# Kernel optimization log

Measured on AMD Instinct MI355X. Metric: run time of the kernel, lower is better.

Reference implementation:

```python
import jax, jax.numpy as jnp
import numpy as np
import math

FEATURE_DIMS = 6
D_HIDDEN = 32
N_TOKENS = 2097152
NUM_SEGMENTS = 8192
SCALE = 400.0 / math.log(10.0)


def setup_inputs() -> dict:
    key = jax.random.key(0)
    ks = jax.random.split(key, 8)
    x = jax.random.normal(ks[0], (N_TOKENS, FEATURE_DIMS), dtype=jnp.float32)
    segment_ids = jnp.sort(jax.random.randint(ks[1], (N_TOKENS,), 0, NUM_SEGMENTS)).astype(jnp.int32)
    # params (kaiming-ish init, same layout as nn.Linear: y = x @ W.T + b -> stored pre-transposed)
    W1 = jax.random.normal(ks[2], (FEATURE_DIMS, D_HIDDEN), dtype=jnp.float32) / np.sqrt(FEATURE_DIMS)
    b1 = jax.random.normal(ks[3], (D_HIDDEN,), dtype=jnp.float32) * 0.01
    wr = jax.random.normal(ks[4], (D_HIDDEN,), dtype=jnp.float32) / np.sqrt(D_HIDDEN)
    br = jax.random.normal(ks[5], (), dtype=jnp.float32) * 0.01
    wz = jax.random.normal(ks[6], (D_HIDDEN,), dtype=jnp.float32) / np.sqrt(D_HIDDEN)
    bz = jax.random.normal(ks[7], (), dtype=jnp.float32) * 0.01
    return {"x": x, "W1": W1, "b1": b1, "wr": wr, "br": br, "wz": wz, "bz": bz,
            "segment_ids": segment_ids, "num_segments": NUM_SEGMENTS}


def reference(x, W1, b1, wr, br, wz, bz, segment_ids, num_segments):
    # layer1: Linear + ReLU  -> h [N, d_hidden]
    h = jax.nn.relu(x @ W1 + b1)
    # rating / weight heads, squeezed to [N]
    r = h @ wr + br
    z = h @ wz + bz
    # per-segment (per-game) softmax over z, weighted sum of r -- single pass, no Python loop
    zmax = jax.ops.segment_max(z, segment_ids, num_segments=num_segments)  # [G], -inf for empty
    e = jnp.exp(z - zmax[segment_ids])                                      # [N]
    num = jax.ops.segment_sum(e * r, segment_ids, num_segments=num_segments)  # [G]
    den = jax.ops.segment_sum(e, segment_ids, num_segments=num_segments)      # [G]
    den_safe = jnp.where(den > 0, den, 1.0)
    preds = jnp.where(den > 0, num / den_safe, 0.0)  # empty segment -> 0, as in the torch code
    return SCALE * preds
```

## Files before the change

kernel.cpp:

```cpp
#include <hip/hip_runtime.h>

#define SCALE_F 173.71779276130078f
#define BLOCK 256
#define TPT 4

typedef float v2f __attribute__((ext_vector_type(2)));

__global__ void zero_ws_kernel(float* __restrict__ ws, int n) {
    int i = blockIdx.x * 256 + threadIdx.x;
    if (i < n) ws[i] = 0.0f;
}

__global__ __launch_bounds__(BLOCK, 8) void strength_main_kernel(
    const float* __restrict__ x,
    const float* __restrict__ W1,
    const float* __restrict__ b1,
    const float* __restrict__ wr,
    const float* __restrict__ brp,
    const float* __restrict__ wz,
    const float* __restrict__ bzp,
    const int*   __restrict__ seg,
    int N,
    float* __restrict__ num,
    float* __restrict__ den)
{
    const int tid  = threadIdx.x;
    const int lane = tid & 63;

    const int t0   = blockIdx.x * (BLOCK * TPT) + tid * TPT;
    const int kmax = (t0 >= N) ? 0 : ((N - t0 < TPT) ? (N - t0) : TPT);

    float a[TPT * 6];
    int   sg[TPT];
    if (kmax == TPT) {
        const float4* xp = (const float4*)(x + (size_t)t0 * 6);
        #pragma unroll
        for (int i = 0; i < 6; ++i) {
            float4 v = xp[i];
            a[4 * i + 0] = v.x; a[4 * i + 1] = v.y;
            a[4 * i + 2] = v.z; a[4 * i + 3] = v.w;
        }
        int4 s0v = *(const int4*)(seg + t0);
        sg[0] = s0v.x; sg[1] = s0v.y; sg[2] = s0v.z; sg[3] = s0v.w;
    } else {
        #pragma unroll
        for (int k = 0; k < TPT; ++k) {
            if (k < kmax) {
                const float* xp = x + (size_t)(t0 + k) * 6;
                #pragma unroll
                for (int i = 0; i < 6; ++i) a[k * 6 + i] = xp[i];
                sg[k] = seg[t0 + k];
            } else {
                #pragma unroll
                for (int i = 0; i < 6; ++i) a[k * 6 + i] = 0.0f;
                sg[k] = -1;
            }
        }
    }

    v2f X[2][6];
    #pragma unroll
    for (int p = 0; p < 2; ++p)
        #pragma unroll
        for (int f = 0; f < 6; ++f)
            X[p][f] = (v2f){ a[(2*p)*6 + f], a[(2*p+1)*6 + f] };

    const float brv = *brp;
    const float bzv = *bzp;

    v2f R[2], Z[2];
    R[0] = (v2f){brv, brv}; R[1] = (v2f){brv, brv};
    Z[0] = (v2f){bzv, bzv}; Z[1] = (v2f){bzv, bzv};

    #pragma unroll 2
    for (int c = 0; c < 16; ++c) {
        const float2 w0 = *(const float2*)&W1[0 * 32 + 2 * c];
        const float2 w1 = *(const float2*)&W1[1 * 32 + 2 * c];
        const float2 w2 = *(const float2*)&W1[2 * 32 + 2 * c];
        const float2 w3 = *(const float2*)&W1[3 * 32 + 2 * c];
        const float2 w4 = *(const float2*)&W1[4 * 32 + 2 * c];
        const float2 w5 = *(const float2*)&W1[5 * 32 + 2 * c];
        const float2 bb = *(const float2*)&b1[2 * c];
        const float2 rr = *(const float2*)&wr[2 * c];
        const float2 zz = *(const float2*)&wz[2 * c];

        #pragma unroll
        for (int j = 0; j < 2; ++j) {
            const float wj0 = j ? w0.y : w0.x;
            const float wj1 = j ? w1.y : w1.x;
            const float wj2 = j ? w2.y : w2.x;
            const float wj3 = j ? w3.y : w3.x;
            const float wj4 = j ? w4.y : w4.x;
            const float wj5 = j ? w5.y : w5.x;
            const float bbj = j ? bb.y : bb.x;
            const float rrj = j ? rr.y : rr.x;
            const float zzj = j ? zz.y : zz.x;
            const v2f vw0 = (v2f){wj0, wj0}, vw1 = (v2f){wj1, wj1};
            const v2f vw2 = (v2f){wj2, wj2}, vw3 = (v2f){wj3, wj3};
            const v2f vw4 = (v2f){wj4, wj4}, vw5 = (v2f){wj5, wj5};
            const v2f vbb = (v2f){bbj, bbj};
            const v2f vrr = (v2f){rrj, rrj}, vzz = (v2f){zzj, zzj};
            #pragma unroll
            for (int p = 0; p < 2; ++p) {
                v2f h = X[p][0]*vw0 + (X[p][1]*vw1 + (X[p][2]*vw2 +
                        (X[p][3]*vw3 + (X[p][4]*vw4 + (X[p][5]*vw5 + vbb)))));
                h = __builtin_elementwise_max(h, (v2f){0.f, 0.f});
                R[p] = h * vrr + R[p];
                Z[p] = h * vzz + Z[p];
            }
        }
    }

    float rv[TPT] = { R[0].x, R[0].y, R[1].x, R[1].y };
    float zv[TPT] = { Z[0].x, Z[0].y, Z[1].x, Z[1].y };

    int   key = (kmax > 0) ? sg[0] : -1;
    float E = 0.0f, ER = 0.0f;
    #pragma unroll
    for (int k = 0; k < TPT; ++k) {
        if (k < kmax) {
            float e = __expf(zv[k]);
            if (sg[k] != key) {
                atomicAdd(&den[key], E);
                atomicAdd(&num[key], ER);
                key = sg[k]; E = 0.0f; ER = 0.0f;
            }
            E += e; ER = fmaf(e, rv[k], ER);
        }
    }

    #pragma unroll
    for (int d = 1; d < 64; d <<= 1) {
        int   k2 = __shfl_up(key, d);
        float E2 = __shfl_up(E,   d);
        float R2 = __shfl_up(ER,  d);
        if (lane >= d && k2 == key) { E += E2; ER += R2; }
    }
    int knext = __shfl_down(key, 1);
    bool last = (lane == 63) || (knext != key);
    if (last && key >= 0) {
        atomicAdd(&den[key], E);
        atomicAdd(&num[key], ER);
    }
}

__global__ void finalize_kernel(const float* __restrict__ num,
                                const float* __restrict__ den,
                                float* __restrict__ out, int G) {
    int g = blockIdx.x * 256 + threadIdx.x;
    if (g < G) {
        float d = den[g];
        out[g] = (d > 0.0f) ? (SCALE_F * num[g] / d) : 0.0f;
    }
}

extern "C" void kernel_launch(void* const* d_in, const int* in_sizes, int n_in,
                              void* d_out, int out_size, void* d_ws, size_t ws_size,
                              hipStream_t stream) {
    const float* x   = (const float*)d_in[0];
    const float* W1  = (const float*)d_in[1];
    const float* b1  = (const float*)d_in[2];
    const float* wr  = (const float*)d_in[3];
    const float* br  = (const float*)d_in[4];
    const float* wz  = (const float*)d_in[5];
    const float* bz  = (const float*)d_in[6];
    const int*   seg = (const int*)d_in[7];

    int N = in_sizes[7];
    int G = out_size;

    float* num = (float*)d_ws;
    float* den = num + G;
    float* out = (float*)d_out;

    int zn = 2 * G;
    zero_ws_kernel<<<(zn + 255) / 256, 256, 0, stream>>>(num, zn);

    long tokens_per_block = (long)BLOCK * TPT;
    int  nblocks = (int)(((long)N + tokens_per_block - 1) / tokens_per_block);
    strength_main_kernel<<<nblocks, BLOCK, 0, stream>>>(
        x, W1, b1, wr, br, wz, bz, seg, N, num, den);

    finalize_kernel<<<(G + 255) / 256, 256, 0, stream>>>(num, den, out, G);
}
```

Before: 28.88 us.

## Stage x through swizzled LDS with coalesced loads and halve tokens per thread

Cuts tokens per thread from four to two, which doubles the number of blocks. Each block now loads its slice of x with fully coalesced float4 reads into XOR-swizzled shared memory, and each thread then reads its own 24-byte rows back from LDS. Before, every thread read its six float4s directly, so accesses across the wavefront were strided. The cost is an added barrier, LDS traffic, and twice as many blocks and segment atomics.

```diff
diff --git a/kernel.cpp b/kernel.cpp
--- a/kernel.cpp
+++ b/kernel.cpp
@@ -2,7 +2,8 @@
 
 #define SCALE_F 173.71779276130078f
 #define BLOCK 256
-#define TPT 4
+#define TPT 2
+#define TOK_PER_BLOCK (BLOCK * TPT)
 
 typedef float v2f __attribute__((ext_vector_type(2)));
 
@@ -10,6 +11,8 @@
     int i = blockIdx.x * 256 + threadIdx.x;
     if (i < n) ws[i] = 0.0f;
 }
+
+__device__ __forceinline__ int swz(int q) { return q ^ ((q >> 3) & 7); }
 
 __global__ __launch_bounds__(BLOCK, 8) void strength_main_kernel(
     const float* __restrict__ x,
@@ -24,25 +27,36 @@
     float* __restrict__ num,
     float* __restrict__ den)
 {
-    const int tid  = threadIdx.x;
-    const int lane = tid & 63;
+    __shared__ float4 xs[TOK_PER_BLOCK * 6 / 4];
 
-    const int t0   = blockIdx.x * (BLOCK * TPT) + tid * TPT;
-    const int kmax = (t0 >= N) ? 0 : ((N - t0 < TPT) ? (N - t0) : TPT);
+    const int tid    = threadIdx.x;
+    const int lane   = tid & 63;
+    const int bstart = blockIdx.x * TOK_PER_BLOCK;
+    const int t0     = bstart + tid * TPT;
 
     float a[TPT * 6];
     int   sg[TPT];
-    if (kmax == TPT) {
-        const float4* xp = (const float4*)(x + (size_t)t0 * 6);
+    int   kmax;
+
+    if (bstart + TOK_PER_BLOCK <= N) {
+        kmax = TPT;
+        const float4* xg = (const float4*)(x + (size_t)bstart * 6);
         #pragma unroll
-        for (int i = 0; i < 6; ++i) {
-            float4 v = xp[i];
-            a[4 * i + 0] = v.x; a[4 * i + 1] = v.y;
-            a[4 * i + 2] = v.z; a[4 * i + 3] = v.w;
+        for (int i = 0; i < 3; ++i) {
+            int q = tid + BLOCK * i;
+            xs[swz(q)] = xg[q];
         }
-        int4 s0v = *(const int4*)(seg + t0);
-        sg[0] = s0v.x; sg[1] = s0v.y; sg[2] = s0v.z; sg[3] = s0v.w;
+        __syncthreads();
+        float4 v0 = xs[swz(3 * tid + 0)];
+        float4 v1 = xs[swz(3 * tid + 1)];
+        float4 v2 = xs[swz(3 * tid + 2)];
+        a[0] = v0.x; a[1]  = v0.y; a[2]  = v0.z; a[3]  = v0.w;
+        a[4] = v1.x; a[5]  = v1.y; a[6]  = v1.z; a[7]  = v1.w;
+        a[8] = v2.x; a[9]  = v2.y; a[10] = v2.z; a[11] = v2.w;
+        int2 s2 = *(const int2*)(seg + t0);
+        sg[0] = s2.x; sg[1] = s2.y;
     } else {
+        kmax = (t0 >= N) ? 0 : ((N - t0 < TPT) ? (N - t0) : TPT);
         #pragma unroll
         for (int k = 0; k < TPT; ++k) {
             if (k < kmax) {
@@ -58,19 +72,15 @@
         }
     }
 
-    v2f X[2][6];
+    v2f X[6];
     #pragma unroll
-    for (int p = 0; p < 2; ++p)
-        #pragma unroll
-        for (int f = 0; f < 6; ++f)
-            X[p][f] = (v2f){ a[(2*p)*6 + f], a[(2*p+1)*6 + f] };
+    for (int f = 0; f < 6; ++f) X[f] = (v2f){ a[f], a[6 + f] };
 
     const float brv = *brp;
     const float bzv = *bzp;
 
-    v2f R[2], Z[2];
-    R[0] = (v2f){brv, brv}; R[1] = (v2f){brv, brv};
-    Z[0] = (v2f){bzv, bzv}; Z[1] = (v2f){bzv, bzv};
+    v2f R = (v2f){brv, brv};
+    v2f Z = (v2f){bzv, bzv};
 
     #pragma unroll 2
     for (int c = 0; c < 16; ++c) {
@@ -100,19 +110,16 @@
             const v2f vw4 = (v2f){wj4, wj4}, vw5 = (v2f){wj5, wj5};
             const v2f vbb = (v2f){bbj, bbj};
             const v2f vrr = (v2f){rrj, rrj}, vzz = (v2f){zzj, zzj};
-            #pragma unroll
-            for (int p = 0; p < 2; ++p) {
-                v2f h = X[p][0]*vw0 + (X[p][1]*vw1 + (X[p][2]*vw2 +
-                        (X[p][3]*vw3 + (X[p][4]*vw4 + (X[p][5]*vw5 + vbb)))));
-                h = __builtin_elementwise_max(h, (v2f){0.f, 0.f});
-                R[p] = h * vrr + R[p];
-                Z[p] = h * vzz + Z[p];
-            }
+            v2f h = X[0]*vw0 + (X[1]*vw1 + (X[2]*vw2 +
+                    (X[3]*vw3 + (X[4]*vw4 + (X[5]*vw5 + vbb)))));
+            h = __builtin_elementwise_max(h, (v2f){0.f, 0.f});
+            R = h * vrr + R;
+            Z = h * vzz + Z;
         }
     }
 
-    float rv[TPT] = { R[0].x, R[0].y, R[1].x, R[1].y };
-    float zv[TPT] = { Z[0].x, Z[0].y, Z[1].x, Z[1].y };
+    float rv[TPT] = { R.x, R.y };
+    float zv[TPT] = { Z.x, Z.y };
 
     int   key = (kmax > 0) ? sg[0] : -1;
     float E = 0.0f, ER = 0.0f;
@@ -176,8 +183,7 @@
     int zn = 2 * G;
     zero_ws_kernel<<<(zn + 255) / 256, 256, 0, stream>>>(num, zn);
 
-    long tokens_per_block = (long)BLOCK * TPT;
-    int  nblocks = (int)(((long)N + tokens_per_block - 1) / tokens_per_block);
+    int nblocks = (int)(((long)N + TOK_PER_BLOCK - 1) / TOK_PER_BLOCK);
     strength_main_kernel<<<nblocks, BLOCK, 0, stream>>>(
         x, W1, b1, wr, br, wz, bz, seg, N, num, den);
 
```

New measurement: 30.89 us. 7.0% more time.

## Fuse finalize into main kernel via last-block ticket and use memset

Applied to the files above, without the earlier changes.

Removes the separate finalize kernel: each block bumps a global ticket counter after its atomics drain, and the last block to finish computes num/den for all segments. The zeroing kernel is replaced by hipMemsetAsync covering the accumulators and the ticket. This saves kernel launches and inter-kernel gaps, but the whole finalize (8192 segments) now runs serially on one block at the tail.

```diff
diff --git a/kernel.cpp b/kernel.cpp
--- a/kernel.cpp
+++ b/kernel.cpp
@@ -5,11 +5,6 @@
 #define TPT 4
 
 typedef float v2f __attribute__((ext_vector_type(2)));
-
-__global__ void zero_ws_kernel(float* __restrict__ ws, int n) {
-    int i = blockIdx.x * 256 + threadIdx.x;
-    if (i < n) ws[i] = 0.0f;
-}
 
 __global__ __launch_bounds__(BLOCK, 8) void strength_main_kernel(
     const float* __restrict__ x,
@@ -20,9 +15,11 @@
     const float* __restrict__ wz,
     const float* __restrict__ bzp,
     const int*   __restrict__ seg,
-    int N,
+    int N, int G, int nblocks,
     float* __restrict__ num,
-    float* __restrict__ den)
+    float* __restrict__ den,
+    int*   __restrict__ ticket,
+    float* __restrict__ out)
 {
     const int tid  = threadIdx.x;
     const int lane = tid & 63;
@@ -142,15 +139,24 @@
         atomicAdd(&den[key], E);
         atomicAdd(&num[key], ER);
     }
-}
 
-__global__ void finalize_kernel(const float* __restrict__ num,
-                                const float* __restrict__ den,
-                                float* __restrict__ out, int G) {
-    int g = blockIdx.x * 256 + threadIdx.x;
-    if (g < G) {
-        float d = den[g];
-        out[g] = (d > 0.0f) ? (SCALE_F * num[g] / d) : 0.0f;
+    __shared__ int isLastS;
+    asm volatile("s_waitcnt vmcnt(0)" ::: "memory");
+    __syncthreads();
+    if (tid == 0) {
+        int t = __hip_atomic_fetch_add(ticket, 1, __ATOMIC_ACQ_REL,
+                                       __HIP_MEMORY_SCOPE_AGENT);
+        isLastS = (t == nblocks - 1) ? 1 : 0;
+    }
+    __syncthreads();
+    if (isLastS) {
+        for (int g = tid; g < G; g += BLOCK) {
+            float d  = __hip_atomic_load(&den[g], __ATOMIC_RELAXED,
+                                         __HIP_MEMORY_SCOPE_AGENT);
+            float nm = __hip_atomic_load(&num[g], __ATOMIC_RELAXED,
+                                         __HIP_MEMORY_SCOPE_AGENT);
+            out[g] = (d > 0.0f) ? (SCALE_F * nm / d) : 0.0f;
+        }
     }
 }
 
@@ -169,17 +175,15 @@
     int N = in_sizes[7];
     int G = out_size;
 
-    float* num = (float*)d_ws;
-    float* den = num + G;
-    float* out = (float*)d_out;
+    float* num    = (float*)d_ws;
+    float* den    = num + G;
+    int*   ticket = (int*)(den + G);
+    float* out    = (float*)d_out;
 
-    int zn = 2 * G;
-    zero_ws_kernel<<<(zn + 255) / 256, 256, 0, stream>>>(num, zn);
+    hipMemsetAsync(num, 0, (size_t)(2 * G + 1) * sizeof(float), stream);
 
     long tokens_per_block = (long)BLOCK * TPT;
     int  nblocks = (int)(((long)N + tokens_per_block - 1) / tokens_per_block);
     strength_main_kernel<<<nblocks, BLOCK, 0, stream>>>(
-        x, W1, b1, wr, br, wz, bz, seg, N, num, den);
-
-    finalize_kernel<<<(G + 255) / 256, 256, 0, stream>>>(num, den, out, G);
+        x, W1, b1, wr, br, wz, bz, seg, N, G, nblocks, num, den, ticket, out);
 }
```

Result: slower. 72.34 us (+150.5%).
